# Kernel tuning notes

Measured on AMD Instinct MI355X. Metric: run time of the kernel, lower is better.

## Reference

```python
import jax, jax.numpy as jnp
import numpy as np

ALPHA = 0.2  # LeakyReLU negative slope
OUT_FEATURES = 64


def dsn2(t):
    # Closed-form doubly-stochastic normalization for one [N, N] slice.
    n = t.shape[0]
    rs = t.sum(axis=1, keepdims=True)          # [N, 1] row sums
    cs = t.sum(axis=0, keepdims=True)          # [1, N] col sums
    lamb = jnp.maximum(rs.max(), cs.max())
    r = n * lamb - t.sum()
    tt = t + (lamb * lamb - lamb * (rs + cs) + rs * cs) / r
    ttm = tt / tt.sum(axis=0)[0]               # divide by first column-sum (scalar), per original
    return jnp.where(t > 0, ttm, t)


def setup_inputs() -> dict:
    key = jax.random.key(0)
    k1, k2, k3, k4 = jax.random.split(key, 4)
    N, P, IN, OUT = 3072, 4, 256, OUT_FEATURES
    h = jax.random.normal(k1, (N, IN), dtype=jnp.float32)
    edge_attr = jax.random.uniform(k2, (P, N, N), dtype=jnp.float32)
    W = jax.random.normal(k3, (IN, OUT), dtype=jnp.float32) * 0.1
    a = jax.random.normal(k4, (2 * OUT, 1), dtype=jnp.float32) * 0.1
    return {"h": h, "edge_attr": edge_attr, "W": W, "a": a}


def reference(h, edge_attr, W, a):
    F = OUT_FEATURES
    Wh = h @ W                                   # [N, F]
    Wh1 = Wh @ a[:F, :]                          # [N, 1]
    Wh2 = Wh @ a[F:, :]                          # [N, 1]
    e = jax.nn.leaky_relu(Wh1 + Wh2.T, negative_slope=ALPHA)  # [N, N]
    e = e * edge_attr                            # [P, N, N]
    attention = jax.vmap(dsn2)(e)                # [P, N, N]
    h_prime = jnp.einsum('pij,jf->pif', attention, Wh)  # [P, N, F]
    # concat=True: cat along feature dim -> [N, P*F]
    N = h.shape[0]
    h_cat = jnp.transpose(h_prime, (1, 0, 2)).reshape(N, -1)
    return jax.nn.elu(h_cat), e
```

## Files before the change

### kernel.cpp

```cpp
#include <hip/hip_runtime.h>
#include <math.h>

#define NN 3072
#define PP 4
#define INF_ 256
#define FF 64
#define LEAK 0.2f
#define KB2 384
#define KS 4
#define KCH (NN / KS)
#define PNF (PP * NN * FF)

#define WH1_OFF  0
#define WH2_OFF  (WH1_OFF + NN)
#define RS_OFF   (WH2_OFF + NN)
#define CS_OFF   (RS_OFF + PP * NN)
#define U_OFF    (CS_OFF + PP * NN)
#define V_OFF    (U_OFF + PP * NN)
#define SCAL_OFF (V_OFF + PP * NN)
#define WHT_OFF  (SCAL_OFF + 8)
#define CP_OFF   (WHT_OFF + (NN * FF) / 2)

typedef short short8 __attribute__((ext_vector_type(8)));
typedef float floatx4 __attribute__((ext_vector_type(4)));

__device__ inline unsigned short f2bf(float x) {
    unsigned u = __float_as_uint(x);
    return (unsigned short)((u + 0x7FFFu + ((u >> 16) & 1u)) >> 16);
}

__global__ __launch_bounds__(64) void k1_gemm(const float* __restrict__ h,
                                              const float* __restrict__ W,
                                              const float* __restrict__ a,
                                              float* __restrict__ ws) {
    int row = blockIdx.x;
    int f = threadIdx.x;
    __shared__ float hrow[INF_];
    ((float4*)hrow)[f] = ((const float4*)(h + (size_t)row * INF_))[f];
    __syncthreads();
    float acc = 0.f;
#pragma unroll 8
    for (int k = 0; k < INF_; ++k) acc = fmaf(hrow[k], W[k * FF + f], acc);
    unsigned short* whT = (unsigned short*)(ws + WHT_OFF);
    whT[(size_t)f * NN + row] = f2bf(acc);
    float s1 = acc * a[f];
    float s2 = acc * a[FF + f];
#pragma unroll
    for (int off = 32; off > 0; off >>= 1) {
        s1 += __shfl_down(s1, off);
        s2 += __shfl_down(s2, off);
    }
    if (f == 0) { ws[WH1_OFF + row] = s1; ws[WH2_OFF + row] = s2; }
}

__global__ __launch_bounds__(256) void k2_e(const float* __restrict__ edge,
                                            float* __restrict__ e_out,
                                            float* __restrict__ ws) {
    int p = blockIdx.y;
    int row0 = blockIdx.x * 8;
    int tid = threadIdx.x;
    const float* Wh1 = ws + WH1_OFF;
    const float4* Wh2v = (const float4*)(ws + WH2_OFF);
    float4 wv[3];
#pragma unroll
    for (int c = 0; c < 3; ++c) wv[c] = Wh2v[c * 256 + tid];
    float colAcc[12];
#pragma unroll
    for (int i = 0; i < 12; ++i) colAcc[i] = 0.f;
    __shared__ float rowpart[8][4];
    const size_t slice = (size_t)p * NN * NN;
#pragma unroll 2
    for (int r = 0; r < 8; ++r) {
        int row = row0 + r;
        float w1 = Wh1[row];
        const float4* ein = (const float4*)(edge + slice + (size_t)row * NN);
        float4* eout = (float4*)(e_out + slice + (size_t)row * NN);
        float racc = 0.f;
#pragma unroll
        for (int c = 0; c < 3; ++c) {
            int j4 = c * 256 + tid;
            float4 ea = ein[j4];
            float4 w = wv[c];
            float4 ev;
            float b;
            b = w1 + w.x; b = b > 0.f ? b : LEAK * b; ev.x = b * ea.x;
            b = w1 + w.y; b = b > 0.f ? b : LEAK * b; ev.y = b * ea.y;
            b = w1 + w.z; b = b > 0.f ? b : LEAK * b; ev.z = b * ea.z;
            b = w1 + w.w; b = b > 0.f ? b : LEAK * b; ev.w = b * ea.w;
            eout[j4] = ev;
            colAcc[c * 4 + 0] += ev.x; colAcc[c * 4 + 1] += ev.y;
            colAcc[c * 4 + 2] += ev.z; colAcc[c * 4 + 3] += ev.w;
            racc += (ev.x + ev.y) + (ev.z + ev.w);
        }
#pragma unroll
        for (int off = 32; off > 0; off >>= 1) racc += __shfl_down(racc, off);
        if ((tid & 63) == 0) rowpart[r][tid >> 6] = racc;
    }
    __syncthreads();
    if (tid < 32) {
        float vv = rowpart[tid >> 2][tid & 3];
        vv += __shfl_down(vv, 2);
        vv += __shfl_down(vv, 1);
        if ((tid & 3) == 0) ws[RS_OFF + p * NN + row0 + (tid >> 2)] = vv;
    }
    float4* cp = (float4*)(ws + CP_OFF + (size_t)(p * KB2 + blockIdx.x) * NN);
#pragma unroll
    for (int c = 0; c < 3; ++c) {
        float4 cv;
        cv.x = colAcc[c * 4 + 0]; cv.y = colAcc[c * 4 + 1];
        cv.z = colAcc[c * 4 + 2]; cv.w = colAcc[c * 4 + 3];
        cp[c * 256 + tid] = cv;
    }
}

__global__ __launch_bounds__(256) void k3a_red(float* __restrict__ ws) {
    int p = blockIdx.y;
    int col = blockIdx.x * 64 + (threadIdx.x & 63);
    int chunk = threadIdx.x >> 6;
    const float* cp = ws + CP_OFF + (size_t)p * KB2 * NN + (size_t)chunk * 96 * NN + col;
    float s = 0.f;
#pragma unroll 8
    for (int b = 0; b < 96; ++b) s += cp[(size_t)b * NN];
    __shared__ float sred[4][64];
    sred[chunk][threadIdx.x & 63] = s;
    __syncthreads();
    if (threadIdx.x < 64) {
        float t = sred[0][threadIdx.x] + sred[1][threadIdx.x] +
                  sred[2][threadIdx.x] + sred[3][threadIdx.x];
        ws[CS_OFF + p * NN + col] = t;
    }
}

__global__ __launch_bounds__(256) void k3b_scal(float* __restrict__ ws) {
    int p = blockIdx.x;
    int tid = threadIdx.x;
    const float* rs = ws + RS_OFF + p * NN;
    const float* cs = ws + CS_OFF + p * NN;
    float mx = -3.4e38f, sum = 0.f;
    for (int i = tid; i < NN; i += 256) {
        float rv = rs[i], cv = cs[i];
        mx = fmaxf(mx, fmaxf(rv, cv));
        sum += rv;
    }
#pragma unroll
    for (int off = 32; off > 0; off >>= 1) {
        mx = fmaxf(mx, __shfl_down(mx, off));
        sum += __shfl_down(sum, off);
    }
    __shared__ float smx[4], ssum[4];
    __shared__ float s_lamb, s_invlr;
    if ((tid & 63) == 0) { smx[tid >> 6] = mx; ssum[tid >> 6] = sum; }
    __syncthreads();
    if (tid == 0) {
        float lamb = fmaxf(fmaxf(smx[0], smx[1]), fmaxf(smx[2], smx[3]));
        float T = ssum[0] + ssum[1] + ssum[2] + ssum[3];
        float r = (float)NN * lamb - T;
        s_lamb = lamb;
        s_invlr = 1.f / (r * lamb);
        ws[SCAL_OFF + p] = 1.f / lamb;
    }
    __syncthreads();
    float lamb = s_lamb, invlr = s_invlr;
    for (int i = tid; i < NN; i += 256) {
        ws[U_OFF + p * NN + i] = (lamb - rs[i]) * invlr;
        ws[V_OFF + p * NN + i] = lamb - cs[i];
    }
}

__global__ __launch_bounds__(64) void k4_mfma(const float* __restrict__ e_in,
                                              float* __restrict__ ws) {
    int p = blockIdx.y;
    int z = blockIdx.z;
    int row0 = blockIdx.x * 16;
    int tid = threadIdx.x;
    __shared__ __align__(16) unsigned short sA[16][56];
    __shared__ __align__(16) unsigned short sB[64][56];
    const unsigned short* whT = (const unsigned short*)(ws + WHT_OFF);
    const float* u = ws + U_OFF + p * NN;
    const float* v = ws + V_OFF + p * NN;
    float invl = ws[SCAL_OFF + p];
    const float* eslice = e_in + (size_t)p * NN * NN;

    int arow = tid >> 2;
    int kg = tid & 3;
    float u_r = u[row0 + arow];
    const float4* erow = (const float4*)(eslice + (size_t)(row0 + arow) * NN);
    const float4* vrow = (const float4*)v;
    const int4* wrow = (const int4*)(whT + (size_t)tid * NN);

    floatx4 acc[4];
#pragma unroll
    for (int nt = 0; nt < 4; ++nt)
#pragma unroll
        for (int i = 0; i < 4; ++i) acc[nt][i] = 0.f;

    const int kbase = z * KCH;
    float4 e0, e1, v0, v1;
    int4 b0, b1, b2, b3;
    auto ldg = [&](int k0) {
        int idx = (k0 >> 2) + kg * 2;
        e0 = erow[idx]; e1 = erow[idx + 1];
        v0 = vrow[idx]; v1 = vrow[idx + 1];
        int widx = k0 >> 3;
        b0 = wrow[widx]; b1 = wrow[widx + 1]; b2 = wrow[widx + 2]; b3 = wrow[widx + 3];
    };
    ldg(kbase);
    for (int k0 = kbase; k0 < kbase + KCH; k0 += 32) {
        float a0 = e0.x > 0.f ? fmaf(u_r, v0.x, e0.x * invl) : e0.x;
        float a1 = e0.y > 0.f ? fmaf(u_r, v0.y, e0.y * invl) : e0.y;
        float a2 = e0.z > 0.f ? fmaf(u_r, v0.z, e0.z * invl) : e0.z;
        float a3 = e0.w > 0.f ? fmaf(u_r, v0.w, e0.w * invl) : e0.w;
        float a4 = e1.x > 0.f ? fmaf(u_r, v1.x, e1.x * invl) : e1.x;
        float a5 = e1.y > 0.f ? fmaf(u_r, v1.y, e1.y * invl) : e1.y;
        float a6 = e1.z > 0.f ? fmaf(u_r, v1.z, e1.z * invl) : e1.z;
        float a7 = e1.w > 0.f ? fmaf(u_r, v1.w, e1.w * invl) : e1.w;
        int4 pa;
        pa.x = (int)f2bf(a0) | ((int)f2bf(a1) << 16);
        pa.y = (int)f2bf(a2) | ((int)f2bf(a3) << 16);
        pa.z = (int)f2bf(a4) | ((int)f2bf(a5) << 16);
        pa.w = (int)f2bf(a6) | ((int)f2bf(a7) << 16);
        *(int4*)&sA[arow][kg * 8] = pa;
        *(int4*)&sB[tid][0]  = b0;
        *(int4*)&sB[tid][8]  = b1;
        *(int4*)&sB[tid][16] = b2;
        *(int4*)&sB[tid][24] = b3;
        __syncthreads();
        if (k0 + 32 < kbase + KCH) ldg(k0 + 32);
        int mrow = tid & 15;
        int kq = tid >> 4;
        short8 af = *(const short8*)&sA[mrow][kq * 8];
#pragma unroll
        for (int nt = 0; nt < 4; ++nt) {
            short8 bf = *(const short8*)&sB[nt * 16 + mrow][kq * 8];
            acc[nt] = __builtin_amdgcn_mfma_f32_16x16x32_bf16(af, bf, acc[nt], 0, 0, 0);
        }
        __syncthreads();
    }
    float* part = ws + CP_OFF + (size_t)z * PNF + (size_t)p * NN * FF + (size_t)row0 * FF;
#pragma unroll
    for (int nt = 0; nt < 4; ++nt)
#pragma unroll
        for (int r = 0; r < 4; ++r)
            part[((tid >> 4) * 4 + r) * FF + nt * 16 + (tid & 15)] = acc[nt][r];
}

__global__ __launch_bounds__(256) void k5_red(const float* __restrict__ ws,
                                              float* __restrict__ out0) {
    int i = blockIdx.x * 256 + threadIdx.x;
    const float* part = ws + CP_OFF;
    float s = part[i] + part[PNF + i] + part[2 * PNF + i] + part[3 * (size_t)PNF + i];
    s = s > 0.f ? s : (expf(s) - 1.0f);
    int f = i & 63;
    int n = (i >> 6) & (NN - 1);
    int p = i >> 6 >> 11;
    p = i / (NN * FF);
    n = (i - p * NN * FF) >> 6;
    out0[(size_t)n * (PP * FF) + p * FF + f] = s;
}

extern "C" void kernel_launch(void* const* d_in, const int* in_sizes, int n_in,
                              void* d_out, int out_size, void* d_ws, size_t ws_size,
                              hipStream_t stream) {
    const float* h    = (const float*)d_in[0];
    const float* edge = (const float*)d_in[1];
    const float* W    = (const float*)d_in[2];
    const float* a    = (const float*)d_in[3];
    float* out0  = (float*)d_out;
    float* e_out = out0 + (size_t)NN * PP * FF;
    float* ws = (float*)d_ws;

    k1_gemm<<<NN, 64, 0, stream>>>(h, W, a, ws);
    k2_e<<<dim3(NN / 8, PP), 256, 0, stream>>>(edge, e_out, ws);
    k3a_red<<<dim3(NN / 64, PP), 256, 0, stream>>>(ws);
    k3b_scal<<<PP, 256, 0, stream>>>(ws);
    k4_mfma<<<dim3(NN / 16, PP, KS), 64, 0, stream>>>(e_out, ws);
    k5_red<<<PNF / 256, 256, 0, stream>>>(ws, out0);
}
```

Baseline: 395.2 us.

## Load MFMA operands directly into registers and use nontemporal e stores

The attention-GEMM kernel no longer stages the A and B tiles through LDS with two barriers per k-step. Each lane now loads its own MFMA fragments straight from global memory, reading e, v and the bf16 Wh^T rows in the fragment layout, and the loop is unrolled by two instead of being software-pipelined explicitly. The e-output write in the edge kernel uses nontemporal stores so the large output stream bypasses the cache. A cleanup of the index math in the reduction kernel is also included. The trade-off is less coalesced global access per wave and reliance on the compiler to hide load latency.

Result: slower. 413.2 us (+4.6%).

```diff
diff --git a/kernel.cpp b/kernel.cpp
--- a/kernel.cpp
+++ b/kernel.cpp
@@ -74,20 +74,20 @@
         int row = row0 + r;
         float w1 = Wh1[row];
         const float4* ein = (const float4*)(edge + slice + (size_t)row * NN);
-        float4* eout = (float4*)(e_out + slice + (size_t)row * NN);
+        float* eoutf = e_out + slice + (size_t)row * NN;
         float racc = 0.f;
 #pragma unroll
         for (int c = 0; c < 3; ++c) {
             int j4 = c * 256 + tid;
             float4 ea = ein[j4];
             float4 w = wv[c];
-            float4 ev;
+            floatx4 ev;
             float b;
             b = w1 + w.x; b = b > 0.f ? b : LEAK * b; ev.x = b * ea.x;
             b = w1 + w.y; b = b > 0.f ? b : LEAK * b; ev.y = b * ea.y;
             b = w1 + w.z; b = b > 0.f ? b : LEAK * b; ev.z = b * ea.z;
             b = w1 + w.w; b = b > 0.f ? b : LEAK * b; ev.w = b * ea.w;
-            eout[j4] = ev;
+            __builtin_nontemporal_store(ev, (floatx4*)(eoutf + (size_t)j4 * 4));
             colAcc[c * 4 + 0] += ev.x; colAcc[c * 4 + 1] += ev.y;
             colAcc[c * 4 + 2] += ev.z; colAcc[c * 4 + 3] += ev.w;
             racc += (ev.x + ev.y) + (ev.z + ev.w);
@@ -173,20 +173,21 @@
     int z = blockIdx.z;
     int row0 = blockIdx.x * 16;
     int tid = threadIdx.x;
-    __shared__ __align__(16) unsigned short sA[16][56];
-    __shared__ __align__(16) unsigned short sB[64][56];
     const unsigned short* whT = (const unsigned short*)(ws + WHT_OFF);
     const float* u = ws + U_OFF + p * NN;
     const float* v = ws + V_OFF + p * NN;
     float invl = ws[SCAL_OFF + p];
     const float* eslice = e_in + (size_t)p * NN * NN;
 
-    int arow = tid >> 2;
-    int kg = tid & 3;
-    float u_r = u[row0 + arow];
-    const float4* erow = (const float4*)(eslice + (size_t)(row0 + arow) * NN);
+    const int mrow = tid & 15;
+    const int kq = tid >> 4;
+    float u_r = u[row0 + mrow];
+    const float4* erow = (const float4*)(eslice + (size_t)(row0 + mrow) * NN);
     const float4* vrow = (const float4*)v;
-    const int4* wrow = (const int4*)(whT + (size_t)tid * NN);
+    const short8* w0 = (const short8*)(whT + (size_t)(0 * 16 + mrow) * NN);
+    const short8* w1 = (const short8*)(whT + (size_t)(1 * 16 + mrow) * NN);
+    const short8* w2 = (const short8*)(whT + (size_t)(2 * 16 + mrow) * NN);
+    const short8* w3 = (const short8*)(whT + (size_t)(3 * 16 + mrow) * NN);
 
     floatx4 acc[4];
 #pragma unroll
@@ -195,17 +196,18 @@
         for (int i = 0; i < 4; ++i) acc[nt][i] = 0.f;
 
     const int kbase = z * KCH;
-    float4 e0, e1, v0, v1;
-    int4 b0, b1, b2, b3;
-    auto ldg = [&](int k0) {
-        int idx = (k0 >> 2) + kg * 2;
-        e0 = erow[idx]; e1 = erow[idx + 1];
-        v0 = vrow[idx]; v1 = vrow[idx + 1];
-        int widx = k0 >> 3;
-        b0 = wrow[widx]; b1 = wrow[widx + 1]; b2 = wrow[widx + 2]; b3 = wrow[widx + 3];
-    };
-    ldg(kbase);
+#pragma unroll 2
     for (int k0 = kbase; k0 < kbase + KCH; k0 += 32) {
+        int ei = (k0 >> 2) + (kq << 1);
+        float4 e0 = erow[ei];
+        float4 e1 = erow[ei + 1];
+        float4 v0 = vrow[ei];
+        float4 v1 = vrow[ei + 1];
+        int wi = (k0 >> 3) + kq;
+        short8 b0 = w0[wi];
+        short8 b1 = w1[wi];
+        short8 b2 = w2[wi];
+        short8 b3 = w3[wi];
         float a0 = e0.x > 0.f ? fmaf(u_r, v0.x, e0.x * invl) : e0.x;
         float a1 = e0.y > 0.f ? fmaf(u_r, v0.y, e0.y * invl) : e0.y;
         float a2 = e0.z > 0.f ? fmaf(u_r, v0.z, e0.z * invl) : e0.z;
@@ -219,22 +221,11 @@
         pa.y = (int)f2bf(a2) | ((int)f2bf(a3) << 16);
         pa.z = (int)f2bf(a4) | ((int)f2bf(a5) << 16);
         pa.w = (int)f2bf(a6) | ((int)f2bf(a7) << 16);
-        *(int4*)&sA[arow][kg * 8] = pa;
-        *(int4*)&sB[tid][0]  = b0;
-        *(int4*)&sB[tid][8]  = b1;
-        *(int4*)&sB[tid][16] = b2;
-        *(int4*)&sB[tid][24] = b3;
-        __syncthreads();
-        if (k0 + 32 < kbase + KCH) ldg(k0 + 32);
-        int mrow = tid & 15;
-        int kq = tid >> 4;
-        short8 af = *(const short8*)&sA[mrow][kq * 8];
-#pragma unroll
-        for (int nt = 0; nt < 4; ++nt) {
-            short8 bf = *(const short8*)&sB[nt * 16 + mrow][kq * 8];
-            acc[nt] = __builtin_amdgcn_mfma_f32_16x16x32_bf16(af, bf, acc[nt], 0, 0, 0);
-        }
-        __syncthreads();
+        short8 af = *(short8*)&pa;
+        acc[0] = __builtin_amdgcn_mfma_f32_16x16x32_bf16(af, b0, acc[0], 0, 0, 0);
+        acc[1] = __builtin_amdgcn_mfma_f32_16x16x32_bf16(af, b1, acc[1], 0, 0, 0);
+        acc[2] = __builtin_amdgcn_mfma_f32_16x16x32_bf16(af, b2, acc[2], 0, 0, 0);
+        acc[3] = __builtin_amdgcn_mfma_f32_16x16x32_bf16(af, b3, acc[3], 0, 0, 0);
     }
     float* part = ws + CP_OFF + (size_t)z * PNF + (size_t)p * NN * FF + (size_t)row0 * FF;
 #pragma unroll
@@ -251,10 +242,8 @@
     float s = part[i] + part[PNF + i] + part[2 * PNF + i] + part[3 * (size_t)PNF + i];
     s = s > 0.f ? s : (expf(s) - 1.0f);
     int f = i & 63;
-    int n = (i >> 6) & (NN - 1);
-    int p = i >> 6 >> 11;
-    p = i / (NN * FF);
-    n = (i - p * NN * FF) >> 6;
+    int p = i / (NN * FF);
+    int n = (i - p * NN * FF) >> 6;
     out0[(size_t)n * (PP * FF) + p * FF + f] = s;
 }
 
```
